# Performance work log

Hardware: AMD Instinct MI355X
Metric: run time of the kernel (lower is better)

The kernel has to match this reference:

```python
import jax, jax.numpy as jnp
import numpy as np


def setup_inputs() -> dict:
    key = jax.random.key(0)
    Y = jax.random.normal(key, (16384, 2048), dtype=jnp.float32)
    return {"Y": Y}


def reference(Y):
    # Original: Y = Y / sqrt(n); D = Y.T @ Y; loss = sum(sqrt((1 - diag(D))**2))
    # diag(Y.T @ Y) == per-column sum of squares -> O(n*d) instead of O(n*d^2)
    n = Y.shape[0]
    Yn = Y / jnp.sqrt(jnp.asarray(n, dtype=Y.dtype))
    diag = jnp.sum(Yn * Yn, axis=0)  # [d]
    loss = jnp.sum(jnp.abs(1.0 - diag))  # sqrt(x**2) == |x|
    return loss
```

## Files before the change

### kernel.cpp

```cpp
#include <hip/hip_runtime.h>

#define NROWS 16384
#define D     2048
#define D4    (D / 4)
#define YBLOCKS 512
#define ROWS_PER_BLOCK (NROWS / YBLOCKS)

__global__ void __launch_bounds__(256)
colsq_partial(const float4* __restrict__ Y4, float4* __restrict__ P4) {
    const int c4 = blockIdx.x * 256 + threadIdx.x;
    const int yb = blockIdx.y;
    const float4* p = Y4 + (size_t)yb * ROWS_PER_BLOCK * D4 + c4;
    float4 acc = make_float4(0.f, 0.f, 0.f, 0.f);
#pragma unroll 8
    for (int r = 0; r < ROWS_PER_BLOCK; ++r) {
        float4 v = p[(size_t)r * D4];
        acc.x += v.x * v.x;
        acc.y += v.y * v.y;
        acc.z += v.z * v.z;
        acc.w += v.w * v.w;
    }
    P4[(size_t)yb * D4 + c4] = acc;
}

__global__ void __launch_bounds__(256)
col_finalize(const float* __restrict__ P, float* __restrict__ ws2) {
    const int col  = blockIdx.x * 64 + (threadIdx.x & 63);
    const int part = threadIdx.x >> 6;
    float s = 0.f;
#pragma unroll 8
    for (int i = 0; i < YBLOCKS / 4; ++i) {
        int yb = part * (YBLOCKS / 4) + i;
        s += P[yb * D + col];
    }
    __shared__ float lds[256];
    lds[threadIdx.x] = s;
    __syncthreads();
    if (threadIdx.x < 64) {
        float tot = lds[threadIdx.x] + lds[threadIdx.x + 64] +
                    lds[threadIdx.x + 128] + lds[threadIdx.x + 192];
        float v = fabsf(1.0f - tot * (1.0f / (float)NROWS));
#pragma unroll
        for (int off = 32; off; off >>= 1)
            v += __shfl_down(v, off, 64);
        if (threadIdx.x == 0) ws2[blockIdx.x] = v;
    }
}

__global__ void __launch_bounds__(64)
final_sum(const float* __restrict__ ws2, float* __restrict__ out) {
    float v = (threadIdx.x < 32) ? ws2[threadIdx.x] : 0.f;
#pragma unroll
    for (int off = 32; off; off >>= 1)
        v += __shfl_down(v, off, 64);
    if (threadIdx.x == 0) out[0] = v;
}

extern "C" void kernel_launch(void* const* d_in, const int* in_sizes, int n_in,
                              void* d_out, int out_size, void* d_ws, size_t ws_size,
                              hipStream_t stream) {
    const float4* Y4 = (const float4*)d_in[0];
    float* out = (float*)d_out;
    float* P   = (float*)d_ws;
    float* ws2 = (float*)((char*)d_ws + (size_t)YBLOCKS * D * sizeof(float));

    colsq_partial<<<dim3(2, YBLOCKS), 256, 0, stream>>>(Y4, (float4*)P);
    col_finalize<<<dim3(32), 256, 0, stream>>>(P, ws2);
    final_sum<<<dim3(1), 64, 0, stream>>>(ws2, out);
}
```

Before: 194.7 us.

## Make each partial block cover all columns with two float4 per thread

Reshapes the partial-sum kernel so each of the 1024 blocks covers the full column width over fewer rows, with each thread loading two float4 per row into separate accumulators. This is meant to give more independent loads in flight per thread. In exchange, the intermediate partial buffer doubles, and the 32-block finalize kernel must read twice as many rows per column.

```diff
diff --git a/kernel.cpp b/kernel.cpp
--- a/kernel.cpp
+++ b/kernel.cpp
@@ -3,24 +3,27 @@
 #define NROWS 16384
 #define D     2048
 #define D4    (D / 4)
-#define YBLOCKS 512
-#define ROWS_PER_BLOCK (NROWS / YBLOCKS)
+#define K1BLOCKS 1024
+#define ROWS_PER_BLOCK (NROWS / K1BLOCKS)
 
 __global__ void __launch_bounds__(256)
 colsq_partial(const float4* __restrict__ Y4, float4* __restrict__ P4) {
-    const int c4 = blockIdx.x * 256 + threadIdx.x;
-    const int yb = blockIdx.y;
-    const float4* p = Y4 + (size_t)yb * ROWS_PER_BLOCK * D4 + c4;
-    float4 acc = make_float4(0.f, 0.f, 0.f, 0.f);
+    const int t = threadIdx.x;
+    const float4* p = Y4 + (size_t)blockIdx.x * ROWS_PER_BLOCK * D4 + t;
+    float4 a0 = make_float4(0.f, 0.f, 0.f, 0.f);
+    float4 a1 = make_float4(0.f, 0.f, 0.f, 0.f);
 #pragma unroll 8
     for (int r = 0; r < ROWS_PER_BLOCK; ++r) {
-        float4 v = p[(size_t)r * D4];
-        acc.x += v.x * v.x;
-        acc.y += v.y * v.y;
-        acc.z += v.z * v.z;
-        acc.w += v.w * v.w;
+        float4 v0 = p[(size_t)r * D4];
+        float4 v1 = p[(size_t)r * D4 + 256];
+        a0.x += v0.x * v0.x;  a0.y += v0.y * v0.y;
+        a0.z += v0.z * v0.z;  a0.w += v0.w * v0.w;
+        a1.x += v1.x * v1.x;  a1.y += v1.y * v1.y;
+        a1.z += v1.z * v1.z;  a1.w += v1.w * v1.w;
     }
-    P4[(size_t)yb * D4 + c4] = acc;
+    float4* q = P4 + (size_t)blockIdx.x * D4;
+    q[t]       = a0;
+    q[t + 256] = a1;
 }
 
 __global__ void __launch_bounds__(256)
@@ -29,9 +32,9 @@
     const int part = threadIdx.x >> 6;
     float s = 0.f;
 #pragma unroll 8
-    for (int i = 0; i < YBLOCKS / 4; ++i) {
-        int yb = part * (YBLOCKS / 4) + i;
-        s += P[yb * D + col];
+    for (int i = 0; i < K1BLOCKS / 4; ++i) {
+        int yb = part * (K1BLOCKS / 4) + i;
+        s += P[(size_t)yb * D + col];
     }
     __shared__ float lds[256];
     lds[threadIdx.x] = s;
@@ -62,9 +65,9 @@
     const float4* Y4 = (const float4*)d_in[0];
     float* out = (float*)d_out;
     float* P   = (float*)d_ws;
-    float* ws2 = (float*)((char*)d_ws + (size_t)YBLOCKS * D * sizeof(float));
+    float* ws2 = (float*)((char*)d_ws + (size_t)K1BLOCKS * D * sizeof(float));
 
-    colsq_partial<<<dim3(2, YBLOCKS), 256, 0, stream>>>(Y4, (float4*)P);
+    colsq_partial<<<dim3(K1BLOCKS), 256, 0, stream>>>(Y4, (float4*)P);
     col_finalize<<<dim3(32), 256, 0, stream>>>(P, ws2);
     final_sum<<<dim3(1), 64, 0, stream>>>(ws2, out);
 }
```

Measured after the change: 202.1 us. +3.8%, slower.

## Use grid-stride sweep for column sums and fuse final reduction via atomic counter

Applied to the files above, without the earlier changes.

The first kernel is restructured so 2048 blocks each walk the whole matrix with a stride of the full grid size. Each thread gets one contiguous float4 per iteration, and all iterations are fully unrolled to keep many loads in flight. The separate final_sum launch is removed: the last finishing block of col_finalize, found through an atomic counter, does the final reduction. This adds a memset and fence or atomic overhead in exchange for one fewer kernel launch.

```diff
diff --git a/kernel.cpp b/kernel.cpp
--- a/kernel.cpp
+++ b/kernel.cpp
@@ -3,57 +3,70 @@
 #define NROWS 16384
 #define D     2048
 #define D4    (D / 4)
-#define YBLOCKS 512
-#define ROWS_PER_BLOCK (NROWS / YBLOCKS)
+#define K1BLK 2048
+#define GSZ   (K1BLK * 256)
+#define ITERS (NROWS * D4 / GSZ)
+#define STRIPES (GSZ / D4)
+#define K2BLK 32
 
 __global__ void __launch_bounds__(256)
-colsq_partial(const float4* __restrict__ Y4, float4* __restrict__ P4) {
-    const int c4 = blockIdx.x * 256 + threadIdx.x;
-    const int yb = blockIdx.y;
-    const float4* p = Y4 + (size_t)yb * ROWS_PER_BLOCK * D4 + c4;
-    float4 acc = make_float4(0.f, 0.f, 0.f, 0.f);
-#pragma unroll 8
-    for (int r = 0; r < ROWS_PER_BLOCK; ++r) {
-        float4 v = p[(size_t)r * D4];
-        acc.x += v.x * v.x;
-        acc.y += v.y * v.y;
-        acc.z += v.z * v.z;
-        acc.w += v.w * v.w;
+colsq_sweep(const float4* __restrict__ Y4, float4* __restrict__ P4) {
+    const int g = blockIdx.x * 256 + threadIdx.x;
+    const float4* p = Y4 + g;
+    float4 a = make_float4(0.f, 0.f, 0.f, 0.f);
+#pragma unroll
+    for (int i = 0; i < ITERS; ++i) {
+        float4 v = p[(size_t)i * GSZ];
+        a.x += v.x * v.x;
+        a.y += v.y * v.y;
+        a.z += v.z * v.z;
+        a.w += v.w * v.w;
     }
-    P4[(size_t)yb * D4 + c4] = acc;
+    P4[g] = a;
 }
 
 __global__ void __launch_bounds__(256)
-col_finalize(const float* __restrict__ P, float* __restrict__ ws2) {
-    const int col  = blockIdx.x * 64 + (threadIdx.x & 63);
-    const int part = threadIdx.x >> 6;
+col_finalize(const float* __restrict__ P, float* __restrict__ ws2,
+             unsigned* __restrict__ counter, float* __restrict__ out) {
+    const int tid  = threadIdx.x;
+    const int col  = blockIdx.x * 64 + (tid & 63);
+    const int part = tid >> 6;
     float s = 0.f;
 #pragma unroll 8
-    for (int i = 0; i < YBLOCKS / 4; ++i) {
-        int yb = part * (YBLOCKS / 4) + i;
-        s += P[yb * D + col];
+    for (int i = 0; i < STRIPES / 4; ++i) {
+        int yb = part * (STRIPES / 4) + i;
+        s += P[(size_t)yb * D + col];
     }
     __shared__ float lds[256];
-    lds[threadIdx.x] = s;
+    lds[tid] = s;
     __syncthreads();
-    if (threadIdx.x < 64) {
-        float tot = lds[threadIdx.x] + lds[threadIdx.x + 64] +
-                    lds[threadIdx.x + 128] + lds[threadIdx.x + 192];
+    if (tid < 64) {
+        float tot = lds[tid] + lds[tid + 64] + lds[tid + 128] + lds[tid + 192];
         float v = fabsf(1.0f - tot * (1.0f / (float)NROWS));
 #pragma unroll
         for (int off = 32; off; off >>= 1)
             v += __shfl_down(v, off, 64);
-        if (threadIdx.x == 0) ws2[blockIdx.x] = v;
+        if (tid == 0) ws2[blockIdx.x] = v;
     }
-}
-
-__global__ void __launch_bounds__(64)
-final_sum(const float* __restrict__ ws2, float* __restrict__ out) {
-    float v = (threadIdx.x < 32) ? ws2[threadIdx.x] : 0.f;
+    __threadfence();
+    __shared__ int is_last;
+    if (tid == 0) {
+        unsigned old = __hip_atomic_fetch_add(counter, 1u, __ATOMIC_ACQ_REL,
+                                              __HIP_MEMORY_SCOPE_AGENT);
+        is_last = (old == K2BLK - 1);
+    }
+    __syncthreads();
+    if (!is_last) return;
+    if (tid < 64) {
+        float v = (tid < K2BLK)
+                    ? __hip_atomic_load(&ws2[tid], __ATOMIC_RELAXED,
+                                        __HIP_MEMORY_SCOPE_AGENT)
+                    : 0.f;
 #pragma unroll
-    for (int off = 32; off; off >>= 1)
-        v += __shfl_down(v, off, 64);
-    if (threadIdx.x == 0) out[0] = v;
+        for (int off = 32; off; off >>= 1)
+            v += __shfl_down(v, off, 64);
+        if (tid == 0) out[0] = v;
+    }
 }
 
 extern "C" void kernel_launch(void* const* d_in, const int* in_sizes, int n_in,
@@ -62,9 +75,10 @@
     const float4* Y4 = (const float4*)d_in[0];
     float* out = (float*)d_out;
     float* P   = (float*)d_ws;
-    float* ws2 = (float*)((char*)d_ws + (size_t)YBLOCKS * D * sizeof(float));
+    float* ws2 = (float*)((char*)d_ws + (size_t)STRIPES * D * sizeof(float));
+    unsigned* counter = (unsigned*)(ws2 + K2BLK);
 
-    colsq_partial<<<dim3(2, YBLOCKS), 256, 0, stream>>>(Y4, (float4*)P);
-    col_finalize<<<dim3(32), 256, 0, stream>>>(P, ws2);
-    final_sum<<<dim3(1), 64, 0, stream>>>(ws2, out);
+    hipMemsetAsync(counter, 0, sizeof(unsigned), stream);
+    colsq_sweep<<<dim3(K1BLK), 256, 0, stream>>>(Y4, (float4*)P);
+    col_finalize<<<dim3(K2BLK), 256, 0, stream>>>(P, ws2, counter, out);
 }
```

After: 209.7 us. +7.7%, slower.
